# Kernel tuning notes

Measured on AMD Instinct MI355X. Metric: run time of the kernel, lower is better.

## Reference

```python
import jax, jax.numpy as jnp
import numpy as np
import math

N, T, V, C = 64, 256, 25, 64  # batch, frames, joints, channels (in==out)
D = C  # out_channels
EPS = 1e-5


def _shift_indices(v, c):
    i = np.arange(v)[:, None]
    j = np.arange(c)[None, :]
    shift_in = ((i * c + j + j * c) % (c * v)).reshape(-1)
    shift_out = ((i * c + j - j * c) % (c * v)).reshape(-1)
    return shift_in.astype(np.int64), shift_out.astype(np.int64)


def setup_inputs() -> dict:
    key = jax.random.key(0)
    k1, k2 = jax.random.split(key)
    si, so = _shift_indices(V, D)
    return {
        "x0": jax.random.normal(k1, (N, T, V, C), dtype=jnp.float32),
        "Linear_weight": jax.random.normal(k2, (C, D), dtype=jnp.float32) * math.sqrt(1.0 / D),
        "Linear_bias": jnp.zeros((1, 1, D), dtype=jnp.float32),
        "Feature_Mask": jnp.zeros((1, V, C), dtype=jnp.float32),
        "gamma": jnp.ones((V * D,), dtype=jnp.float32),
        "beta": jnp.zeros((V * D,), dtype=jnp.float32),
        "shift_in": jnp.asarray(si),
        "shift_out": jnp.asarray(so),
    }


def reference(x0, Linear_weight, Linear_bias, Feature_Mask, gamma, beta, shift_in, shift_out):
    n, t, v, c = x0.shape
    d = Linear_weight.shape[1]
    # shift-in gather over flattened (node, channel) axis
    x = x0.reshape(n * t, v * c)[:, shift_in].reshape(n * t, v, c)
    # learned feature mask (tanh + 1)
    x = x * (jnp.tanh(Feature_Mask) + 1.0)
    # pointwise channel transform + bias
    x = jnp.einsum('nwc,cd->nwd', x, Linear_weight) + Linear_bias
    # shift-out gather
    x = x.reshape(n * t, v * d)[:, shift_out]
    # BatchNorm1d (training mode): batch stats over n*t rows, biased var
    mean = jnp.mean(x, axis=0)
    var = jnp.var(x, axis=0)
    x = (x - mean) * (gamma / jnp.sqrt(var + EPS)) + beta
    # residual (in_channels == out_channels -> identity down) + ReLU
    y = jax.nn.relu(x.reshape(n, t, v, d) + x0)
    # original returns (n, out_channels, t, v)
    return jnp.transpose(y, (0, 3, 1, 2))
```

## Files before the change

### kernel.cpp

```cpp
#include <hip/hip_runtime.h>
#include <math.h>


typedef __attribute__((ext_vector_type(8))) short bf16x8;
typedef __attribute__((ext_vector_type(4))) float f32x4;

__device__ __forceinline__ ushort f2bf(float f) {
  uint u; __builtin_memcpy(&u, &f, 4);
  u += 0x7fffu + ((u >> 16) & 1u);
  return (ushort)(u >> 16);
}
__device__ __forceinline__ float bf2f(ushort b) {
  uint u = ((uint)b) << 16; float f; __builtin_memcpy(&f, &u, 4); return f;
}

__global__ void k_prep(const float* __restrict__ mask, float* __restrict__ ws) {
  int i = blockIdx.x * 256 + threadIdx.x;
  if (i < 1600) {
    int w = i >> 6, c = i & 63;
    int wr = (w + c) % 25;
    ((ushort*)ws)[wr * 64 + c] = f2bf(tanhf(mask[i]) + 1.0f);
  }
  if (i < 3200) ws[1600 + i] = 0.0f;
}

__global__ void k_finalize(const float* __restrict__ gamma,
                           const float* __restrict__ beta,
                           float* __restrict__ ws) {
  int q = blockIdx.x * 256 + threadIdx.x;
  if (q >= 1600) return;
  const float inv = 1.0f / 16384.0f;
  float mean = ws[1600 + q] * inv;
  float var  = ws[3200 + q] * inv - mean * mean;
  float istd = rsqrtf(var + 1e-5f);
  int w = q >> 6, d = q & 63;
  int p = ((w + d) % 25) * 64 + d;
  float mul = gamma[p] * istd;
  ws[4800 + q] = mul;
  ws[6400 + q] = beta[p] - mean * mul;
}

template<int PASS>
__launch_bounds__(256, 4)
__global__ void k_main(const float* __restrict__ x0,
                       const float* __restrict__ Wg,
                       float* ws,
                       float* __restrict__ out) {
  __shared__ __align__(8)  ushort s_maskm[1600];
  __shared__ __align__(16) ushort s_A[4096];
  __shared__ float s_raw[PASS == 2 ? 3400 : 4];
  __shared__ float s_aux[3200];

  const int tid = threadIdx.x;
  const int lr  = tid & 63;
  const int wid = tid >> 6;

  for (int i = tid; i < 800; i += 256)
    ((uint*)s_maskm)[i] = ((const uint*)ws)[i];
  for (int i = tid; i < 2048; i += 256)
    ((uint*)s_A)[i] = 0u;

  bf16x8 wfrag[2][4];
  #pragma unroll
  for (int ks = 0; ks < 2; ++ks)
    #pragma unroll
    for (int nt = 0; nt < 4; ++nt) {
      const int d = nt * 16 + (lr & 15);
      const int cb = ks * 32 + (lr >> 4) * 8;
      #pragma unroll
      for (int j = 0; j < 8; ++j)
        wfrag[ks][nt][j] = (short)f2bf(Wg[(cb + j) * 64 + d]);
    }

  float cmul[16], cadd[16];
  float ssum[16], ssq[16];
  #pragma unroll
  for (int k = 0; k < 16; ++k) { ssum[k] = 0.f; ssq[k] = 0.f; }
  if constexpr (PASS == 2) {
    #pragma unroll
    for (int nt = 0; nt < 4; ++nt)
      #pragma unroll
      for (int r = 0; r < 4; ++r) {
        int row = wid * 16 + (lr >> 4) * 4 + r;
        int w = row & 31;
        int d = nt * 16 + (lr & 15);
        int qq = (w < 25) ? (w * 64 + d) : 0;
        cmul[nt * 4 + r] = ws[4800 + qq];
        cadd[nt * 4 + r] = ws[6400 + qq];
      }
  }

  const int row_base = blockIdx.x * 16;
  const int n  = row_base >> 8;
  const int t0 = row_base & 255;

  if constexpr (PASS == 1) {
    for (int i = tid; i < 3200; i += 256) s_aux[i] = 0.f;
  }
  __syncthreads();

  for (int rp = 0; rp < 16; rp += 2) {
    const float* xrow = x0 + (size_t)(row_base + rp) * 1600;

    for (int i4 = tid; i4 < 800; i4 += 256) {
      float4 v = ((const float4*)xrow)[i4];
      int r2 = (i4 >= 400) ? 1 : 0;
      int p4 = (i4 - r2 * 400) * 4;
      int wr = p4 >> 6, c0 = p4 & 63;
      if constexpr (PASS == 2)
        *(float4*)&s_raw[r2 * 1700 + wr * 68 + c0] = v;
      uint2 mm = *(const uint2*)&s_maskm[p4];
      float va[4] = {v.x, v.y, v.z, v.w};
      float ma[4] = {bf2f((ushort)(mm.x & 0xffff)), bf2f((ushort)(mm.x >> 16)),
                     bf2f((ushort)(mm.y & 0xffff)), bf2f((ushort)(mm.y >> 16))};
      int wbase = wr + 100 - c0;
      #pragma unroll
      for (int j = 0; j < 4; ++j) {
        int w = (wbase - j) % 25;
        int row = r2 * 32 + w;
        int byte = (row * 128 + (c0 + j) * 2) ^ ((w & 7) << 4);
        *(ushort*)((char*)s_A + byte) = f2bf(va[j] * ma[j]);
      }
    }
    __syncthreads();

    const int arow = wid * 16 + (lr & 15);
    bf16x8 afrag[2];
    #pragma unroll
    for (int ks = 0; ks < 2; ++ks) {
      int byte = (arow * 128 + ks * 64 + (lr >> 4) * 16) ^ ((arow & 7) << 4);
      afrag[ks] = *(const bf16x8*)((const char*)s_A + byte);
    }
    f32x4 acc[4];
    #pragma unroll
    for (int nt = 0; nt < 4; ++nt) {
      acc[nt] = (f32x4){0.f, 0.f, 0.f, 0.f};
      #pragma unroll
      for (int ks = 0; ks < 2; ++ks)
        acc[nt] = __builtin_amdgcn_mfma_f32_16x16x32_bf16(afrag[ks], wfrag[ks][nt], acc[nt], 0, 0, 0);
    }

    if constexpr (PASS == 1) {
      #pragma unroll
      for (int nt = 0; nt < 4; ++nt)
        #pragma unroll
        for (int r = 0; r < 4; ++r) {
          float y = acc[nt][r];
          ssum[nt * 4 + r] += y;
          ssq [nt * 4 + r]  = fmaf(y, y, ssq[nt * 4 + r]);
        }
      __syncthreads();
    } else {
      #pragma unroll
      for (int nt = 0; nt < 4; ++nt)
        #pragma unroll
        for (int r = 0; r < 4; ++r) {
          int row = wid * 16 + (lr >> 4) * 4 + r;
          int r2 = row >> 5;
          int w  = row & 31;
          if (w < 25) {
            int d  = nt * 16 + (lr & 15);
            int wp = (w + d) % 25;
            float y = fmaf(acc[nt][r], cmul[nt * 4 + r], cadd[nt * 4 + r]);
            y += s_raw[r2 * 1700 + wp * 68 + d];
            s_aux[d * 50 + r2 * 25 + wp] = fmaxf(y, 0.f);
          }
        }
      __syncthreads();
      const size_t obase = (size_t)n * 409600 + (size_t)(t0 + rp) * 25;
      for (int i = tid; i < 3200; i += 256) {
        int d   = i / 50;
        int rem = i - d * 50;
        int r2  = rem / 25;
        int wp  = rem - r2 * 25;
        out[obase + (size_t)d * 6400 + r2 * 25 + wp] = s_aux[i];
      }
      __syncthreads();
    }
  }

  if constexpr (PASS == 1) {
    #pragma unroll
    for (int nt = 0; nt < 4; ++nt)
      #pragma unroll
      for (int r = 0; r < 4; ++r) {
        int row = wid * 16 + (lr >> 4) * 4 + r;
        int w = row & 31;
        if (w < 25) {
          int q = w * 64 + nt * 16 + (lr & 15);
          atomicAdd(&s_aux[q],        ssum[nt * 4 + r]);
          atomicAdd(&s_aux[1600 + q], ssq [nt * 4 + r]);
        }
      }
    __syncthreads();
    for (int i = tid; i < 3200; i += 256)
      atomicAdd(&ws[1600 + i], s_aux[i]);
  }
}

extern "C" void kernel_launch(void* const* d_in, const int* in_sizes, int n_in,
                              void* d_out, int out_size, void* d_ws, size_t ws_size,
                              hipStream_t stream) {
  const float* x0    = (const float*)d_in[0];
  const float* W     = (const float*)d_in[1];
  const float* mask  = (const float*)d_in[3];
  const float* gamma = (const float*)d_in[4];
  const float* beta  = (const float*)d_in[5];
  float* ws  = (float*)d_ws;
  float* out = (float*)d_out;

  k_prep    <<<13,   256, 0, stream>>>(mask, ws);
  k_main<1> <<<1024, 256, 0, stream>>>(x0, W, ws, out);
  k_finalize<<<7,    256, 0, stream>>>(gamma, beta, ws);
  k_main<2> <<<1024, 256, 0, stream>>>(x0, W, ws, out);
}
```

Baseline: 346.7 us.

## Prefetch next x0 row pair into registers and replicate BN stat accumulators

The main kernel now loads the next two rows of x0 into registers while the current pair is converted and multiplied, so global load latency overlaps with the LDS writes and MFMA work. The pass-1 statistics are also spread over 64 replicated global accumulators chosen by block index, cutting atomic contention on a single 3200-float buffer. The finalize kernel sums the 64 replicas, and the prep kernel zeroes the larger area with more blocks. The cost is higher register pressure from eight float4 staging registers, plus extra workspace and reduction work in finalize.

```diff
diff --git a/kernel.cpp b/kernel.cpp
--- a/kernel.cpp
+++ b/kernel.cpp
@@ -21,7 +21,8 @@
     int wr = (w + c) % 25;
     ((ushort*)ws)[wr * 64 + c] = f2bf(tanhf(mask[i]) + 1.0f);
   }
-  if (i < 3200) ws[1600 + i] = 0.0f;
+  for (int j = 8000 + i; j < 8000 + 64 * 3200; j += gridDim.x * 256)
+    ws[j] = 0.0f;
 }
 
 __global__ void k_finalize(const float* __restrict__ gamma,
@@ -29,9 +30,15 @@
                            float* __restrict__ ws) {
   int q = blockIdx.x * 256 + threadIdx.x;
   if (q >= 1600) return;
+  float sum = 0.f, sq = 0.f;
+  #pragma unroll 4
+  for (int s = 0; s < 64; ++s) {
+    sum += ws[8000 + s * 3200 + q];
+    sq  += ws[8000 + s * 3200 + 1600 + q];
+  }
   const float inv = 1.0f / 16384.0f;
-  float mean = ws[1600 + q] * inv;
-  float var  = ws[3200 + q] * inv - mean * mean;
+  float mean = sum * inv;
+  float var  = sq * inv - mean * mean;
   float istd = rsqrtf(var + 1e-5f);
   int w = q >> 6, d = q & 63;
   int p = ((w + d) % 25) * 64 + d;
@@ -99,11 +106,19 @@
   }
   __syncthreads();
 
+  float4 cur0, cur1, cur2, cur3, nxt0, nxt1, nxt2, nxt3;
+  {
+    const float4* p = (const float4*)(x0 + (size_t)row_base * 1600);
+    cur0 = p[tid]; cur1 = p[tid + 256]; cur2 = p[tid + 512];
+    if (tid < 32) cur3 = p[tid + 768];
+  }
+
   for (int rp = 0; rp < 16; rp += 2) {
-    const float* xrow = x0 + (size_t)(row_base + rp) * 1600;
-
-    for (int i4 = tid; i4 < 800; i4 += 256) {
-      float4 v = ((const float4*)xrow)[i4];
+    #pragma unroll
+    for (int s = 0; s < 4; ++s) {
+      if (s == 3 && tid >= 32) break;
+      int i4 = (s < 3) ? (tid + s * 256) : (768 + tid);
+      float4 v = (s == 0) ? cur0 : (s == 1) ? cur1 : (s == 2) ? cur2 : cur3;
       int r2 = (i4 >= 400) ? 1 : 0;
       int p4 = (i4 - r2 * 400) * 4;
       int wr = p4 >> 6, c0 = p4 & 63;
@@ -121,6 +136,12 @@
         int byte = (row * 128 + (c0 + j) * 2) ^ ((w & 7) << 4);
         *(ushort*)((char*)s_A + byte) = f2bf(va[j] * ma[j]);
       }
+    }
+
+    if (rp + 2 < 16) {
+      const float4* p = (const float4*)(x0 + (size_t)(row_base + rp + 2) * 1600);
+      nxt0 = p[tid]; nxt1 = p[tid + 256]; nxt2 = p[tid + 512];
+      if (tid < 32) nxt3 = p[tid + 768];
     }
     __syncthreads();
 
@@ -177,6 +198,11 @@
       }
       __syncthreads();
     }
+
+    if (rp + 2 < 16) {
+      cur0 = nxt0; cur1 = nxt1; cur2 = nxt2;
+      if (tid < 32) cur3 = nxt3;
+    }
   }
 
   if constexpr (PASS == 1) {
@@ -193,8 +219,9 @@
         }
       }
     __syncthreads();
+    float* rep = ws + 8000 + (blockIdx.x & 63) * 3200;
     for (int i = tid; i < 3200; i += 256)
-      atomicAdd(&ws[1600 + i], s_aux[i]);
+      atomicAdd(&rep[i], s_aux[i]);
   }
 }
 
@@ -209,7 +236,7 @@
   float* ws  = (float*)d_ws;
   float* out = (float*)d_out;
 
-  k_prep    <<<13,   256, 0, stream>>>(mask, ws);
+  k_prep    <<<200,  256, 0, stream>>>(mask, ws);
   k_main<1> <<<1024, 256, 0, stream>>>(x0, W, ws, out);
   k_finalize<<<7,    256, 0, stream>>>(gamma, beta, ws);
   k_main<2> <<<1024, 256, 0, stream>>>(x0, W, ws, out);
```

New measurement: 368.5 us. 1.06x slower.
